# Optimization experiments

Measured on AMD Instinct MI355X. Metric: run time of the kernel, lower is better.

Reference implementation:

```python
import jax, jax.numpy as jnp
import numpy as np

B, S, D_IN, D_OUT = 4, 2048, 4096, 4096
E = 32        # n_loras (number of LoRA experts)
R = 16        # per-expert rank; E*R == rmoe == 512
K = 2         # top_k
SCALING = 32.0 / 16.0  # lora_alpha / r (use_rslora=False)


def setup_inputs() -> dict:
    key = jax.random.key(0)
    ks = jax.random.split(key, 5)
    x = jax.random.normal(ks[0], (B, S, D_IN), dtype=jnp.float32)
    base_w = jax.random.normal(ks[1], (D_OUT, D_IN), dtype=jnp.float32) * 0.02
    gate_w = jax.random.normal(ks[2], (E, D_IN), dtype=jnp.float32) * 0.02
    lora_A = jax.random.normal(ks[3], (E * R, D_IN), dtype=jnp.float32) * 0.02
    lora_B = jax.random.normal(ks[4], (D_OUT, E * R), dtype=jnp.float32) * 0.02
    return {"x": x, "base_w": base_w, "gate_w": gate_w, "lora_A": lora_A, "lora_B": lora_B}


def reference(x, base_w, gate_w, lora_A, lora_B):
    # Base linear layer (nn.Linear, no bias)
    base = jnp.einsum('bsd,od->bso', x, base_w)

    # Gating: softmax over n_loras experts, top-k selection, renormalize
    logits = jnp.einsum('bsd,ed->bse', x, gate_w)              # [B,S,E]
    probs = jax.nn.softmax(logits, axis=-1)
    vals, idx = jax.lax.top_k(probs, K)                         # [B,S,K]
    vals = vals / jnp.sum(vals, axis=-1, keepdims=True)
    # Dense per-expert weight (zero for unselected experts)
    w = jnp.sum(jax.nn.one_hot(idx, E, dtype=x.dtype) * vals[..., None], axis=-2)  # [B,S,E]

    # Shared stacked LoRA: lora_A rows / lora_B cols are per-expert rank-R blocks
    ax = jnp.einsum('bsd,rd->bsr', x, lora_A).reshape(B, S, E, R)   # [B,S,E,R]
    b_blk = lora_B.T.reshape(E, R, D_OUT)                           # [E,R,out]
    delta = jnp.einsum('bser,ero->bso', ax * w[..., None], b_blk) * SCALING

    return base + delta
```

## Files before the change

kernel.cpp:

```cpp
#include <hip/hip_runtime.h>


#define D_IN   4096
#define D_OUT  4096
#define NTOK   8192
#define NE     32
#define RMOE   512
#define KCAT   4608
#define SCALING 2.0f

typedef unsigned short u16;
typedef __attribute__((ext_vector_type(4))) float  f32x4;
typedef __attribute__((ext_vector_type(4))) unsigned short u16x4;
typedef __attribute__((ext_vector_type(8))) short  bf16x8;

__device__ __forceinline__ u16 f2bf(float f) {
  unsigned u = __float_as_uint(f);
  u += 0x7FFFu + ((u >> 16) & 1u);
  return (u16)(u >> 16);
}

__device__ __forceinline__ void gload16(const void* g, void* l) {
  __builtin_amdgcn_global_load_lds(
      (const __attribute__((address_space(1))) unsigned*)g,
      (__attribute__((address_space(3))) unsigned*)l, 16, 0, 0);
}

#define BAR() do { asm volatile("" ::: "memory"); \
                   __builtin_amdgcn_s_barrier();  \
                   asm volatile("" ::: "memory"); } while (0)
#define WAITV4() asm volatile("s_waitcnt vmcnt(4)" ::: "memory")
#define WAITV0() asm volatile("s_waitcnt vmcnt(0)" ::: "memory")

#define TT 32
#define KC 256
#define LPAD (KC + 4)

__global__ __launch_bounds__(256) void k_logits(
    const float* __restrict__ x, const float* __restrict__ gate_w,
    float* __restrict__ wdense, u16* __restrict__ xb)
{
  __shared__ float smem[2 * TT * LPAD];
  __shared__ int   e1s[TT]; __shared__ int   e2s[TT];
  __shared__ float w1s[TT]; __shared__ float w2s[TT];
  float* xs = smem;
  float* gs = smem + TT * LPAD;

  const int tid  = threadIdx.x;
  const int lane = tid & 63, wave = tid >> 6;
  const int tg = lane >> 3, eg = lane & 7;
  const int row0 = blockIdx.x * TT;
  const int kb = wave * 64;

  float acc[4][4];
#pragma unroll
  for (int t = 0; t < 4; ++t)
#pragma unroll
    for (int e = 0; e < 4; ++e) acc[t][e] = 0.f;

  for (int kt = 0; kt < D_IN / KC; ++kt) {
    __syncthreads();
#pragma unroll
    for (int i = 0; i < 8; ++i) {
      int c = tid + i * 256;
      int tok = c >> 6, kq = c & 63;
      f32x4 v = ((const f32x4*)(x + (size_t)(row0 + tok) * D_IN + kt * KC))[kq];
      *(f32x4*)&xs[tok * LPAD + kq * 4] = v;
      u16x4 h;
      h[0] = f2bf(v[0]); h[1] = f2bf(v[1]); h[2] = f2bf(v[2]); h[3] = f2bf(v[3]);
      ((u16x4*)(xb + (size_t)(row0 + tok) * KCAT + kt * KC))[kq] = h;
    }
#pragma unroll
    for (int i = 0; i < 8; ++i) {
      int c = tid + i * 256;
      int e = c >> 6, kq = c & 63;
      f32x4 v = ((const f32x4*)(gate_w + (size_t)e * D_IN + kt * KC))[kq];
      *(f32x4*)&gs[e * LPAD + kq * 4] = v;
    }
    __syncthreads();
#pragma unroll 4
    for (int kk = 0; kk < 64; kk += 4) {
      f32x4 xv[4], gv[4];
#pragma unroll
      for (int t = 0; t < 4; ++t)
        xv[t] = *(const f32x4*)&xs[(tg * 4 + t) * LPAD + kb + kk];
#pragma unroll
      for (int e = 0; e < 4; ++e)
        gv[e] = *(const f32x4*)&gs[(eg * 4 + e) * LPAD + kb + kk];
#pragma unroll
      for (int t = 0; t < 4; ++t)
#pragma unroll
        for (int e = 0; e < 4; ++e)
#pragma unroll
          for (int m = 0; m < 4; ++m)
            acc[t][e] += xv[t][m] * gv[e][m];
    }
  }

  __syncthreads();
  float* red = smem;
#pragma unroll
  for (int t = 0; t < 4; ++t)
#pragma unroll
    for (int e = 0; e < 4; ++e)
      red[(wave * 64 + lane) * 16 + t * 4 + e] = acc[t][e];
  __syncthreads();
  float* lgt = smem + 4096;
  if (wave == 0) {
#pragma unroll
    for (int i = 0; i < 16; ++i) {
      float s = red[(0 * 64 + lane) * 16 + i] + red[(1 * 64 + lane) * 16 + i]
              + red[(2 * 64 + lane) * 16 + i] + red[(3 * 64 + lane) * 16 + i];
      int t = i >> 2, e = i & 3;
      lgt[(tg * 4 + t) * 36 + eg * 4 + e] = s;
    }
  }
  __syncthreads();
  if (tid < TT) {
    float l1 = -1e30f; int e1 = 0;
    for (int e = 0; e < NE; ++e) { float v = lgt[tid * 36 + e]; if (v > l1) { l1 = v; e1 = e; } }
    float l2 = -1e30f; int e2 = 0;
    for (int e = 0; e < NE; ++e) { if (e == e1) continue; float v = lgt[tid * 36 + e]; if (v > l2) { l2 = v; e2 = e; } }
    float t = __expf(l2 - l1);
    float w2 = t / (1.f + t);
    e1s[tid] = e1; e2s[tid] = e2; w1s[tid] = 1.f - w2; w2s[tid] = w2;
  }
  __syncthreads();
#pragma unroll
  for (int i = 0; i < 4; ++i) {
    int c = tid + i * 256;
    int tok = c >> 5, e = c & 31;
    float v = (e == e1s[tok]) ? w1s[tok] : (e == e2s[tok]) ? w2s[tok] : 0.f;
    wdense[(size_t)(row0 + tok) * NE + e] = v;
  }
}

__global__ __launch_bounds__(256) void k_wconv(
    const float* __restrict__ base_w, const float* __restrict__ lora_B,
    const float* __restrict__ lora_A, u16* __restrict__ wb, u16* __restrict__ la)
{
  const int bid = blockIdx.x, tid = threadIdx.x;
  if (bid < D_OUT) {
    const float* src = base_w + (size_t)bid * D_IN;
    u16* dst = wb + (size_t)bid * KCAT;
#pragma unroll
    for (int i = 0; i < 4; ++i) {
      int c = tid + i * 256;
      f32x4 v = ((const f32x4*)src)[c];
      u16x4 h; h[0] = f2bf(v[0]); h[1] = f2bf(v[1]); h[2] = f2bf(v[2]); h[3] = f2bf(v[3]);
      ((u16x4*)dst)[c] = h;
    }
    if (tid < 128) {
      f32x4 v = ((const f32x4*)(lora_B + (size_t)bid * RMOE))[tid];
      u16x4 h; h[0] = f2bf(v[0]); h[1] = f2bf(v[1]); h[2] = f2bf(v[2]); h[3] = f2bf(v[3]);
      ((u16x4*)(dst + D_IN))[tid] = h;
    }
  } else {
    int r = bid - D_OUT;
    const float* src = lora_A + (size_t)r * D_IN;
    u16* dst = la + (size_t)r * D_IN;
#pragma unroll
    for (int i = 0; i < 4; ++i) {
      int c = tid + i * 256;
      f32x4 v = ((const f32x4*)src)[c];
      u16x4 h; h[0] = f2bf(v[0]); h[1] = f2bf(v[1]); h[2] = f2bf(v[2]); h[3] = f2bf(v[3]);
      ((u16x4*)dst)[c] = h;
    }
  }
}

__global__ __launch_bounds__(256) void k_gemm_ax(
    const u16* __restrict__ A, const u16* __restrict__ Bw,
    const float* __restrict__ wdense, u16* __restrict__ xb)
{
  __shared__ u16 As[128 * 64];
  __shared__ u16 Bs[128 * 64];
  const int nbx = RMOE / 128;
  const int nwg = gridDim.x;
  int bid = blockIdx.x;
  int wg = (bid & 7) * (nwg >> 3) + (bid >> 3);
  const int tm = wg / nbx, tn = wg % nbx;
  const int tid = threadIdx.x;
  const int lane = tid & 63, wave = tid >> 6;
  const int wr = wave >> 1, wc = wave & 1;

  f32x4 acc[4][4];
#pragma unroll
  for (int i = 0; i < 4; ++i)
#pragma unroll
    for (int j = 0; j < 4; ++j) acc[i][j] = (f32x4){0.f, 0.f, 0.f, 0.f};

  const int row0 = tm * 128, col0 = tn * 128;
  for (int kt = 0; kt < D_IN / 64; ++kt) {
    __syncthreads();
#pragma unroll
    for (int i = 0; i < 4; ++i) {
      int c = tid + i * 256;
      int r = c >> 3, c8 = c & 7;
      gload16(A  + (size_t)(row0 + r) * KCAT + kt * 64 + c8 * 8, &As[c * 8]);
      gload16(Bw + (size_t)(col0 + r) * D_IN + kt * 64 + c8 * 8, &Bs[c * 8]);
    }
    __syncthreads();
#pragma unroll
    for (int kk = 0; kk < 2; ++kk) {
      bf16x8 af[4], bfr[4];
      int ko = kk * 32 + (lane >> 4) * 8;
#pragma unroll
      for (int i = 0; i < 4; ++i) {
        af[i]  = *(const bf16x8*)&As[(wr * 64 + i * 16 + (lane & 15)) * 64 + ko];
        bfr[i] = *(const bf16x8*)&Bs[(wc * 64 + i * 16 + (lane & 15)) * 64 + ko];
      }
#pragma unroll
      for (int i = 0; i < 4; ++i)
#pragma unroll
        for (int j = 0; j < 4; ++j)
          acc[i][j] = __builtin_amdgcn_mfma_f32_16x16x32_bf16(af[i], bfr[j], acc[i][j], 0, 0, 0);
    }
  }
#pragma unroll
  for (int i = 0; i < 4; ++i) {
    int rbase = row0 + wr * 64 + i * 16 + ((lane >> 4) << 2);
#pragma unroll
    for (int j = 0; j < 4; ++j) {
      int cb = col0 + wc * 64 + j * 16 + (lane & 15);
#pragma unroll
      for (int q = 0; q < 4; ++q) {
        int trow = rbase + q;
        float wgt = wdense[(size_t)trow * NE + (cb >> 4)];
        xb[(size_t)trow * KCAT + D_IN + cb] = f2bf(acc[i][j][q] * wgt * SCALING);
      }
    }
  }
}

#define NT (KCAT / 64)

__global__ __launch_bounds__(512, 2) void k_gemm_main(
    const u16* __restrict__ A, const u16* __restrict__ Bw, float* __restrict__ C)
{
  __shared__ u16 sh[65536];

  const int tid  = threadIdx.x;
  const int lane = tid & 63;
  const int wv   = tid >> 6;
  const int wm   = wv >> 2;
  const int wn   = wv & 3;
  const int l15  = lane & 15, g = lane >> 4;

  const int nwg = gridDim.x;
  int bid = blockIdx.x;
  int wg = (bid & 7) * (nwg >> 3) + (bid >> 3);
  const int tn = wg & 15, tm = wg >> 4;

  const int rsw   = (g ^ (l15 & 7)) * 8;
  const int aBase = l15 * 64 + rsw;
  const int bBase = ((wn & 1) * 64 + l15) * 64 + rsw;

  const int c0 = tid, c1 = tid + 512;
  const int r0s = c0 >> 3, s0s = (c0 & 7) ^ (r0s & 7);
  const int r1s = c1 >> 3, s1s = (c1 & 7) ^ (r1s & 7);
  const size_t offc0 = (size_t)r0s * KCAT + s0s * 8;
  const size_t offc1 = (size_t)r1s * KCAT + s1s * 8;
  const u16* pA0a = A  + (size_t)(tm * 256 +   0) * KCAT + offc0;
  const u16* pA0b = A  + (size_t)(tm * 256 +   0) * KCAT + offc1;
  const u16* pA1a = A  + (size_t)(tm * 256 + 128) * KCAT + offc0;
  const u16* pA1b = A  + (size_t)(tm * 256 + 128) * KCAT + offc1;
  const u16* pB0a = Bw + (size_t)(tn * 256 +   0) * KCAT + offc0;
  const u16* pB0b = Bw + (size_t)(tn * 256 +   0) * KCAT + offc1;
  const u16* pB1a = Bw + (size_t)(tn * 256 + 128) * KCAT + offc0;
  const u16* pB1b = Bw + (size_t)(tn * 256 + 128) * KCAT + offc1;
  const int d0 = c0 * 8, d1 = c1 * 8;

#define STG(pa, pb, base) do { \
    gload16((pa), &sh[(base) + d0]); \
    gload16((pb), &sh[(base) + d1]); \
    (pa) += 64; (pb) += 64; } while (0)

  f32x4 acc[8][4];
#pragma unroll
  for (int i = 0; i < 8; ++i)
#pragma unroll
    for (int j = 0; j < 4; ++j) acc[i][j] = (f32x4){0.f, 0.f, 0.f, 0.f};

  STG(pA0a, pA0b,     0);
  STG(pB0a, pB0b, 16384);
  STG(pA1a, pA1b,  8192);
  STG(pB1a, pB1b, 24576);
  STG(pA0a, pA0b, 32768 +     0);
  STG(pB0a, pB0b, 32768 + 16384);
  WAITV4();
  BAR();

  bf16x8 aLo[4][2], aHi[4][2], bR[2][2];

  for (int u = 0; u < NT; ++u) {
    const int cb = (u & 1) << 15;
    const int nb = cb ^ 32768;
    const int shA = cb + (wm << 13);
    const int shB = cb + 16384 + ((wn >> 1) << 13);

    if (u < NT - 1) STG(pA1a, pA1b, nb + 8192);
#pragma unroll
    for (int m = 0; m < 4; ++m) {
      int ix = shA + aBase + m * 1024;
      aLo[m][0] = *(const bf16x8*)&sh[ix];
      aLo[m][1] = *(const bf16x8*)&sh[ix ^ 32];
    }
#pragma unroll
    for (int n = 0; n < 2; ++n) {
      int ix = shB + bBase + n * 1024;
      bR[n][0] = *(const bf16x8*)&sh[ix];
      bR[n][1] = *(const bf16x8*)&sh[ix ^ 32];
    }
    BAR();
    __builtin_amdgcn_s_setprio(1);
#pragma unroll
    for (int m = 0; m < 4; ++m)
#pragma unroll
      for (int n = 0; n < 2; ++n)
#pragma unroll
        for (int kk = 0; kk < 2; ++kk)
          acc[m][n] = __builtin_amdgcn_mfma_f32_16x16x32_bf16(aLo[m][kk], bR[n][kk], acc[m][n], 0, 0, 0);
    __builtin_amdgcn_s_setprio(0);
    BAR();

    if (u < NT - 1) STG(pB1a, pB1b, nb + 24576);
#pragma unroll
    for (int m = 0; m < 4; ++m) {
      int ix = shA + aBase + (m + 4) * 1024;
      aHi[m][0] = *(const bf16x8*)&sh[ix];
      aHi[m][1] = *(const bf16x8*)&sh[ix ^ 32];
    }
    BAR();
    __builtin_amdgcn_s_setprio(1);
#pragma unroll
    for (int m = 0; m < 4; ++m)
#pragma unroll
      for (int n = 0; n < 2; ++n)
#pragma unroll
        for (int kk = 0; kk < 2; ++kk)
          acc[m + 4][n] = __builtin_amdgcn_mfma_f32_16x16x32_bf16(aHi[m][kk], bR[n][kk], acc[m + 4][n], 0, 0, 0);
    __builtin_amdgcn_s_setprio(0);
    BAR();

    if (u < NT - 2) STG(pA0a, pA0b, cb + 0);
#pragma unroll
    for (int n = 0; n < 2; ++n) {
      int ix = shB + bBase + (n + 2) * 1024;
      bR[n][0] = *(const bf16x8*)&sh[ix];
      bR[n][1] = *(const bf16x8*)&sh[ix ^ 32];
    }
    BAR();
    __builtin_amdgcn_s_setprio(1);
#pragma unroll
    for (int m = 0; m < 4; ++m)
#pragma unroll
      for (int n = 0; n < 2; ++n)
#pragma unroll
        for (int kk = 0; kk < 2; ++kk)
          acc[m + 4][n + 2] = __builtin_amdgcn_mfma_f32_16x16x32_bf16(aHi[m][kk], bR[n][kk], acc[m + 4][n + 2], 0, 0, 0);
    __builtin_amdgcn_s_setprio(0);
    BAR();

    if (u < NT - 2) { STG(pB0a, pB0b, cb + 16384); WAITV4(); }
    else            { WAITV0(); }
    BAR();
    __builtin_amdgcn_s_setprio(1);
#pragma unroll
    for (int m = 0; m < 4; ++m)
#pragma unroll
      for (int n = 0; n < 2; ++n)
#pragma unroll
        for (int kk = 0; kk < 2; ++kk)
          acc[m][n + 2] = __builtin_amdgcn_mfma_f32_16x16x32_bf16(aLo[m][kk], bR[n][kk], acc[m][n + 2], 0, 0, 0);
    __builtin_amdgcn_s_setprio(0);
    BAR();
  }
#undef STG

  const int crow0 = tm * 256 + wm * 128 + g * 4;
  const int ccol0 = tn * 256 + wn * 64 + l15;
#pragma unroll
  for (int mf = 0; mf < 8; ++mf)
#pragma unroll
    for (int n = 0; n < 4; ++n)
#pragma unroll
      for (int q = 0; q < 4; ++q)
        C[(size_t)(crow0 + mf * 16 + q) * D_OUT + ccol0 + n * 16] = acc[mf][n][q];
}

extern "C" void kernel_launch(void* const* d_in, const int* in_sizes, int n_in,
                              void* d_out, int out_size, void* d_ws, size_t ws_size,
                              hipStream_t stream) {
  const float* x      = (const float*)d_in[0];
  const float* base_w = (const float*)d_in[1];
  const float* gate_w = (const float*)d_in[2];
  const float* lora_A = (const float*)d_in[3];
  const float* lora_B = (const float*)d_in[4];
  float* out = (float*)d_out;

  char* ws = (char*)d_ws;
  u16* xb       = (u16*)ws;
  u16* wb       = (u16*)(ws + 75497472);
  u16* la       = (u16*)(ws + 75497472 + 37748736);
  float* wdense = (float*)(ws + 75497472 + 37748736 + 4194304);

  hipLaunchKernelGGL(k_logits,    dim3(NTOK / TT),    dim3(256), 0, stream, x, gate_w, wdense, xb);
  hipLaunchKernelGGL(k_wconv,     dim3(D_OUT + RMOE), dim3(256), 0, stream, base_w, lora_B, lora_A, wb, la);
  hipLaunchKernelGGL(k_gemm_ax,   dim3((NTOK/128) * (RMOE/128)),  dim3(256), 0, stream, xb, la, wdense, xb);
  hipLaunchKernelGGL(k_gemm_main, dim3((NTOK/256) * (D_OUT/256)), dim3(512), 0, stream, xb, wb, out);
}
```

Measured before the change: 435.2 us.

## Pipeline all three GEMM stages with swizzled LDS and prefetched fragments

The gating-logit kernel gets a larger 8x8 register tile per thread, an XOR-swizzled LDS layout in place of padding, and a cross-lane shuffle reduction. The LoRA-A GEMM moves from synchronous single-buffered loads to a triple-buffered async global-to-LDS pipeline with swizzled fragment reads and fewer barriers. The main GEMM reorders its phases so that the next tile's A/B fragments are read from LDS at the end of each iteration, overlapping LDS reads with MFMA work. The aim is to cut LDS bank conflicts and load latency stalls, at the cost of more registers and LDS per block, which may lower occupancy.

```diff
diff --git a/kernel.cpp b/kernel.cpp
--- a/kernel.cpp
+++ b/kernel.cpp
@@ -29,34 +29,35 @@
 #define BAR() do { asm volatile("" ::: "memory"); \
                    __builtin_amdgcn_s_barrier();  \
                    asm volatile("" ::: "memory"); } while (0)
+#define WAITV8() asm volatile("s_waitcnt vmcnt(8)" ::: "memory")
 #define WAITV4() asm volatile("s_waitcnt vmcnt(4)" ::: "memory")
 #define WAITV0() asm volatile("s_waitcnt vmcnt(0)" ::: "memory")
 
 #define TT 32
 #define KC 256
-#define LPAD (KC + 4)
 
 __global__ __launch_bounds__(256) void k_logits(
     const float* __restrict__ x, const float* __restrict__ gate_w,
     float* __restrict__ wdense, u16* __restrict__ xb)
 {
-  __shared__ float smem[2 * TT * LPAD];
+  __shared__ float smem[2 * TT * KC];
+  __shared__ float lgt[TT * 36];
   __shared__ int   e1s[TT]; __shared__ int   e2s[TT];
   __shared__ float w1s[TT]; __shared__ float w2s[TT];
   float* xs = smem;
-  float* gs = smem + TT * LPAD;
+  float* gs = smem + TT * KC;
 
   const int tid  = threadIdx.x;
   const int lane = tid & 63, wave = tid >> 6;
-  const int tg = lane >> 3, eg = lane & 7;
+  const int ks = lane >> 4, tg = (lane >> 2) & 3, eg = lane & 3;
   const int row0 = blockIdx.x * TT;
-  const int kb = wave * 64;
-
-  float acc[4][4];
-#pragma unroll
-  for (int t = 0; t < 4; ++t)
-#pragma unroll
-    for (int e = 0; e < 4; ++e) acc[t][e] = 0.f;
+  const int kc0 = wave * 16 + ks * 4;
+
+  float acc[8][8];
+#pragma unroll
+  for (int t = 0; t < 8; ++t)
+#pragma unroll
+    for (int e = 0; e < 8; ++e) acc[t][e] = 0.f;
 
   for (int kt = 0; kt < D_IN / KC; ++kt) {
     __syncthreads();
@@ -65,7 +66,7 @@
       int c = tid + i * 256;
       int tok = c >> 6, kq = c & 63;
       f32x4 v = ((const f32x4*)(x + (size_t)(row0 + tok) * D_IN + kt * KC))[kq];
-      *(f32x4*)&xs[tok * LPAD + kq * 4] = v;
+      *(f32x4*)&xs[tok * KC + ((kq ^ (tok >> 3)) << 2)] = v;
       u16x4 h;
       h[0] = f2bf(v[0]); h[1] = f2bf(v[1]); h[2] = f2bf(v[2]); h[3] = f2bf(v[3]);
       ((u16x4*)(xb + (size_t)(row0 + tok) * KCAT + kt * KC))[kq] = h;
@@ -75,45 +76,57 @@
       int c = tid + i * 256;
       int e = c >> 6, kq = c & 63;
       f32x4 v = ((const f32x4*)(gate_w + (size_t)e * D_IN + kt * KC))[kq];
-      *(f32x4*)&gs[e * LPAD + kq * 4] = v;
+      *(f32x4*)&gs[e * KC + ((kq ^ (e >> 3)) << 2)] = v;
     }
     __syncthreads();
-#pragma unroll 4
-    for (int kk = 0; kk < 64; kk += 4) {
-      f32x4 xv[4], gv[4];
-#pragma unroll
-      for (int t = 0; t < 4; ++t)
-        xv[t] = *(const f32x4*)&xs[(tg * 4 + t) * LPAD + kb + kk];
-#pragma unroll
-      for (int e = 0; e < 4; ++e)
-        gv[e] = *(const f32x4*)&gs[(eg * 4 + e) * LPAD + kb + kk];
-#pragma unroll
-      for (int t = 0; t < 4; ++t)
-#pragma unroll
-        for (int e = 0; e < 4; ++e)
+#pragma unroll
+    for (int j = 0; j < 4; ++j) {
+      const int Kc = kc0 + j;
+      f32x4 xv[8], gv[8];
+#pragma unroll
+      for (int t = 0; t < 8; ++t)
+        xv[t] = *(const f32x4*)&xs[(tg * 8 + t) * KC + ((Kc ^ tg) << 2)];
+#pragma unroll
+      for (int e = 0; e < 8; ++e)
+        gv[e] = *(const f32x4*)&gs[(eg * 8 + e) * KC + ((Kc ^ eg) << 2)];
+#pragma unroll
+      for (int t = 0; t < 8; ++t)
+#pragma unroll
+        for (int e = 0; e < 8; ++e)
 #pragma unroll
           for (int m = 0; m < 4; ++m)
             acc[t][e] += xv[t][m] * gv[e][m];
     }
   }
 
+#pragma unroll
+  for (int t = 0; t < 8; ++t)
+#pragma unroll
+    for (int e = 0; e < 8; ++e) {
+      float v = acc[t][e];
+      v += __shfl_xor(v, 16);
+      v += __shfl_xor(v, 32);
+      acc[t][e] = v;
+    }
   __syncthreads();
   float* red = smem;
-#pragma unroll
-  for (int t = 0; t < 4; ++t)
-#pragma unroll
-    for (int e = 0; e < 4; ++e)
-      red[(wave * 64 + lane) * 16 + t * 4 + e] = acc[t][e];
+  if (ks == 0) {
+#pragma unroll
+    for (int t = 0; t < 8; ++t)
+#pragma unroll
+      for (int e4 = 0; e4 < 8; e4 += 4) {
+        f32x4 v = { acc[t][e4], acc[t][e4 + 1], acc[t][e4 + 2], acc[t][e4 + 3] };
+        *(f32x4*)&red[(wave * 16 + tg * 4 + eg) * 64 + t * 8 + e4] = v;
+      }
+  }
   __syncthreads();
-  float* lgt = smem + 4096;
-  if (wave == 0) {
-#pragma unroll
-    for (int i = 0; i < 16; ++i) {
-      float s = red[(0 * 64 + lane) * 16 + i] + red[(1 * 64 + lane) * 16 + i]
-              + red[(2 * 64 + lane) * 16 + i] + red[(3 * 64 + lane) * 16 + i];
-      int t = i >> 2, e = i & 3;
-      lgt[(tg * 4 + t) * 36 + eg * 4 + e] = s;
-    }
+  {
+    int tok = tid >> 3, e4 = (tid & 7) << 2;
+    f32x4 s = {0.f, 0.f, 0.f, 0.f};
+#pragma unroll
+    for (int w = 0; w < 4; ++w)
+      s += *(const f32x4*)&red[(w * 16 + (tok >> 3) * 4 + (e4 >> 3)) * 64 + (tok & 7) * 8 + (e4 & 7)];
+    *(f32x4*)&lgt[tok * 36 + e4] = s;
   }
   __syncthreads();
   if (tid < TT) {
@@ -173,8 +186,7 @@
     const u16* __restrict__ A, const u16* __restrict__ Bw,
     const float* __restrict__ wdense, u16* __restrict__ xb)
 {
-  __shared__ u16 As[128 * 64];
-  __shared__ u16 Bs[128 * 64];
+  __shared__ u16 sh[49152];
   const int nbx = RMOE / 128;
   const int nwg = gridDim.x;
   int bid = blockIdx.x;
@@ -183,6 +195,23 @@
   const int tid = threadIdx.x;
   const int lane = tid & 63, wave = tid >> 6;
   const int wr = wave >> 1, wc = wave & 1;
+  const int l15 = lane & 15, g = lane >> 4;
+  const int row0 = tm * 128, col0 = tn * 128;
+
+  size_t offA[4], offB[4]; int dstd[4];
+#pragma unroll
+  for (int i = 0; i < 4; ++i) {
+    int c = tid + i * 256;
+    int r = c >> 3, s = (c & 7) ^ (r & 7);
+    offA[i] = (size_t)(row0 + r) * KCAT + s * 8;
+    offB[i] = (size_t)(col0 + r) * D_IN + s * 8;
+    dstd[i] = c * 8;
+  }
+
+#define STGAX(b, kt) do { \
+    _Pragma("unroll") for (int i = 0; i < 4; ++i) { \
+      gload16(A  + offA[i] + (size_t)(kt) * 64, &sh[(b) * 16384 + dstd[i]]); \
+      gload16(Bw + offB[i] + (size_t)(kt) * 64, &sh[(b) * 16384 + 8192 + dstd[i]]); } } while (0)
 
   f32x4 acc[4][4];
 #pragma unroll
@@ -190,39 +219,44 @@
 #pragma unroll
     for (int j = 0; j < 4; ++j) acc[i][j] = (f32x4){0.f, 0.f, 0.f, 0.f};
 
-  const int row0 = tm * 128, col0 = tn * 128;
+  STGAX(0, 0);
+  STGAX(1, 1);
+  WAITV8();
+  BAR();
+
+  const int swz = (g ^ (l15 & 7)) * 8;
   for (int kt = 0; kt < D_IN / 64; ++kt) {
-    __syncthreads();
+    if (kt + 2 < D_IN / 64) STGAX((kt + 2) % 3, kt + 2);
+    const u16* As_ = &sh[(kt % 3) * 16384];
+    const u16* Bs_ = &sh[(kt % 3) * 16384 + 8192];
+    bf16x8 af[4][2], bfr[4][2];
 #pragma unroll
     for (int i = 0; i < 4; ++i) {
-      int c = tid + i * 256;
-      int r = c >> 3, c8 = c & 7;
-      gload16(A  + (size_t)(row0 + r) * KCAT + kt * 64 + c8 * 8, &As[c * 8]);
-      gload16(Bw + (size_t)(col0 + r) * D_IN + kt * 64 + c8 * 8, &Bs[c * 8]);
-    }
-    __syncthreads();
-#pragma unroll
-    for (int kk = 0; kk < 2; ++kk) {
-      bf16x8 af[4], bfr[4];
-      int ko = kk * 32 + (lane >> 4) * 8;
-#pragma unroll
-      for (int i = 0; i < 4; ++i) {
-        af[i]  = *(const bf16x8*)&As[(wr * 64 + i * 16 + (lane & 15)) * 64 + ko];
-        bfr[i] = *(const bf16x8*)&Bs[(wc * 64 + i * 16 + (lane & 15)) * 64 + ko];
-      }
-#pragma unroll
-      for (int i = 0; i < 4; ++i)
-#pragma unroll
-        for (int j = 0; j < 4; ++j)
-          acc[i][j] = __builtin_amdgcn_mfma_f32_16x16x32_bf16(af[i], bfr[j], acc[i][j], 0, 0, 0);
-    }
-  }
+      int ixa = (wr * 64 + i * 16 + l15) * 64 + swz;
+      af[i][0] = *(const bf16x8*)&As_[ixa]; af[i][1] = *(const bf16x8*)&As_[ixa ^ 32];
+      int ixb = (wc * 64 + i * 16 + l15) * 64 + swz;
+      bfr[i][0] = *(const bf16x8*)&Bs_[ixb]; bfr[i][1] = *(const bf16x8*)&Bs_[ixb ^ 32];
+    }
+    __builtin_amdgcn_s_setprio(1);
+#pragma unroll
+    for (int i = 0; i < 4; ++i)
+#pragma unroll
+      for (int j = 0; j < 4; ++j)
+#pragma unroll
+        for (int kk = 0; kk < 2; ++kk)
+          acc[i][j] = __builtin_amdgcn_mfma_f32_16x16x32_bf16(af[i][kk], bfr[j][kk], acc[i][j], 0, 0, 0);
+    __builtin_amdgcn_s_setprio(0);
+    if (kt >= D_IN / 64 - 2) WAITV0(); else WAITV8();
+    BAR();
+  }
+#undef STGAX
+
 #pragma unroll
   for (int i = 0; i < 4; ++i) {
-    int rbase = row0 + wr * 64 + i * 16 + ((lane >> 4) << 2);
+    int rbase = row0 + wr * 64 + i * 16 + (g << 2);
 #pragma unroll
     for (int j = 0; j < 4; ++j) {
-      int cb = col0 + wc * 64 + j * 16 + (lane & 15);
+      int cb = col0 + wc * 64 + j * 16 + l15;
 #pragma unroll
       for (int q = 0; q < 4; ++q) {
         int trow = rbase + q;
@@ -276,6 +310,13 @@
     gload16((pb), &sh[(base) + d1]); \
     (pa) += 64; (pb) += 64; } while (0)
 
+#define MM4x2(MO, NO, AF, BF) do { \
+    _Pragma("unroll") for (int m_ = 0; m_ < 4; ++m_) \
+    _Pragma("unroll") for (int n_ = 0; n_ < 2; ++n_) \
+    _Pragma("unroll") for (int kk_ = 0; kk_ < 2; ++kk_) \
+      acc[m_ + (MO)][n_ + (NO)] = __builtin_amdgcn_mfma_f32_16x16x32_bf16( \
+          AF[m_][kk_], BF[n_][kk_], acc[m_ + (MO)][n_ + (NO)], 0, 0, 0); } while (0)
+
   f32x4 acc[8][4];
 #pragma unroll
   for (int i = 0; i < 8; ++i)
@@ -291,74 +332,58 @@
   WAITV4();
   BAR();
 
-  bf16x8 aLo[4][2], aHi[4][2], bR[2][2];
+  bf16x8 aA[4][2], aB[4][2], bR[2][2];
+  {
+    const int shA = (wm << 13);
+    const int shB = 16384 + ((wn >> 1) << 13);
+#pragma unroll
+    for (int m = 0; m < 4; ++m) {
+      int ix = shA + aBase + m * 1024;
+      aA[m][0] = *(const bf16x8*)&sh[ix]; aA[m][1] = *(const bf16x8*)&sh[ix ^ 32];
+    }
+#pragma unroll
+    for (int n = 0; n < 2; ++n) {
+      int ix = shB + bBase + n * 1024;
+      bR[n][0] = *(const bf16x8*)&sh[ix]; bR[n][1] = *(const bf16x8*)&sh[ix ^ 32];
+    }
+  }
 
   for (int u = 0; u < NT; ++u) {
     const int cb = (u & 1) << 15;
     const int nb = cb ^ 32768;
-    const int shA = cb + (wm << 13);
-    const int shB = cb + 16384 + ((wn >> 1) << 13);
+    const int shA  = cb + (wm << 13);
+    const int shB  = cb + 16384 + ((wn >> 1) << 13);
+    const int shAn = nb + (wm << 13);
+    const int shBn = nb + 16384 + ((wn >> 1) << 13);
 
     if (u < NT - 1) STG(pA1a, pA1b, nb + 8192);
-#pragma unroll
-    for (int m = 0; m < 4; ++m) {
-      int ix = shA + aBase + m * 1024;
-      aLo[m][0] = *(const bf16x8*)&sh[ix];
-      aLo[m][1] = *(const bf16x8*)&sh[ix ^ 32];
-    }
-#pragma unroll
-    for (int n = 0; n < 2; ++n) {
-      int ix = shB + bBase + n * 1024;
-      bR[n][0] = *(const bf16x8*)&sh[ix];
-      bR[n][1] = *(const bf16x8*)&sh[ix ^ 32];
-    }
-    BAR();
-    __builtin_amdgcn_s_setprio(1);
-#pragma unroll
-    for (int m = 0; m < 4; ++m)
-#pragma unroll
-      for (int n = 0; n < 2; ++n)
-#pragma unroll
-        for (int kk = 0; kk < 2; ++kk)
-          acc[m][n] = __builtin_amdgcn_mfma_f32_16x16x32_bf16(aLo[m][kk], bR[n][kk], acc[m][n], 0, 0, 0);
-    __builtin_amdgcn_s_setprio(0);
-    BAR();
-
-    if (u < NT - 1) STG(pB1a, pB1b, nb + 24576);
 #pragma unroll
     for (int m = 0; m < 4; ++m) {
       int ix = shA + aBase + (m + 4) * 1024;
-      aHi[m][0] = *(const bf16x8*)&sh[ix];
-      aHi[m][1] = *(const bf16x8*)&sh[ix ^ 32];
+      aB[m][0] = *(const bf16x8*)&sh[ix]; aB[m][1] = *(const bf16x8*)&sh[ix ^ 32];
     }
     BAR();
     __builtin_amdgcn_s_setprio(1);
-#pragma unroll
-    for (int m = 0; m < 4; ++m)
-#pragma unroll
-      for (int n = 0; n < 2; ++n)
-#pragma unroll
-        for (int kk = 0; kk < 2; ++kk)
-          acc[m + 4][n] = __builtin_amdgcn_mfma_f32_16x16x32_bf16(aHi[m][kk], bR[n][kk], acc[m + 4][n], 0, 0, 0);
+    MM4x2(0, 0, aA, bR);
     __builtin_amdgcn_s_setprio(0);
     BAR();
 
-    if (u < NT - 2) STG(pA0a, pA0b, cb + 0);
+    if (u < NT - 1) STG(pB1a, pB1b, nb + 24576);
+    BAR();
+    __builtin_amdgcn_s_setprio(1);
+    MM4x2(4, 0, aB, bR);
+    __builtin_amdgcn_s_setprio(0);
 #pragma unroll
     for (int n = 0; n < 2; ++n) {
       int ix = shB + bBase + (n + 2) * 1024;
-      bR[n][0] = *(const bf16x8*)&sh[ix];
-      bR[n][1] = *(const bf16x8*)&sh[ix ^ 32];
-    }
+      bR[n][0] = *(const bf16x8*)&sh[ix]; bR[n][1] = *(const bf16x8*)&sh[ix ^ 32];
+    }
+    BAR();
+
+    if (u < NT - 2) STG(pA0a, pA0b, cb + 0);
     BAR();
     __builtin_amdgcn_s_setprio(1);
-#pragma unroll
-    for (int m = 0; m < 4; ++m)
-#pragma unroll
-      for (int n = 0; n < 2; ++n)
-#pragma unroll
-        for (int kk = 0; kk < 2; ++kk)
-          acc[m + 4][n + 2] = __builtin_amdgcn_mfma_f32_16x16x32_bf16(aHi[m][kk], bR[n][kk], acc[m + 4][n + 2], 0, 0, 0);
+    MM4x2(4, 2, aB, bR);
     __builtin_amdgcn_s_setprio(0);
     BAR();
 
@@ -366,17 +391,24 @@
     else            { WAITV0(); }
     BAR();
     __builtin_amdgcn_s_setprio(1);
-#pragma unroll
-    for (int m = 0; m < 4; ++m)
-#pragma unroll
-      for (int n = 0; n < 2; ++n)
-#pragma unroll
-        for (int kk = 0; kk < 2; ++kk)
-          acc[m][n + 2] = __builtin_amdgcn_mfma_f32_16x16x32_bf16(aLo[m][kk], bR[n][kk], acc[m][n + 2], 0, 0, 0);
+    MM4x2(0, 2, aA, bR);
     __builtin_amdgcn_s_setprio(0);
+    if (u < NT - 1) {
+#pragma unroll
+      for (int m = 0; m < 4; ++m) {
+        int ix = shAn + aBase + m * 1024;
+        aA[m][0] = *(const bf16x8*)&sh[ix]; aA[m][1] = *(const bf16x8*)&sh[ix ^ 32];
+      }
+#pragma unroll
+      for (int n = 0; n < 2; ++n) {
+        int ix = shBn + bBase + n * 1024;
+        bR[n][0] = *(const bf16x8*)&sh[ix]; bR[n][1] = *(const bf16x8*)&sh[ix ^ 32];
+      }
+    }
     BAR();
   }
 #undef STG
+#undef MM4x2
 
   const int crow0 = tm * 256 + wm * 128 + g * 4;
   const int ccol0 = tn * 256 + wn * 64 + l15;
```

Measured after the change: 384.3 us. -11.7%, faster.
